# Optimization experiments

Hardware: AMD Instinct MI355X
Metric: run time of the kernel (lower is better)

Reference implementation:

```python
import jax, jax.numpy as jnp
import numpy as np

N, E, D = 8192, 4096, 256
EDGE_DENSITY = 0.05  # ~410 nodes per hyperedge; guarantees no empty edge


def _layernorm(x, gamma, beta, eps=1e-5):
    mu = jnp.mean(x, axis=-1, keepdims=True)
    var = jnp.mean((x - mu) ** 2, axis=-1, keepdims=True)
    return (x - mu) * jax.lax.rsqrt(var + eps) * gamma + beta


def setup_inputs() -> dict:
    key = jax.random.key(0)
    k1, k2, k3 = jax.random.split(key, 3)
    node_embeddings = jax.random.normal(k1, (N, D), dtype=jnp.float32)
    # scale 1/sqrt(N) keeps two chained NxN matmuls per layer numerically sane
    target_martrix = jax.random.normal(k2, (N, N), dtype=jnp.float32) / np.float32(np.sqrt(N))
    hypergraph_matrix = (jax.random.uniform(k3, (N, E)) < EDGE_DENSITY).astype(jnp.float32)
    ln_gamma = jnp.ones((D,), jnp.float32)
    ln_beta = jnp.zeros((D,), jnp.float32)
    return {
        "node_embeddings": node_embeddings,
        "target_martrix": target_martrix,
        "hypergraph_matrix": hypergraph_matrix,
        "ln_gamma": ln_gamma,
        "ln_beta": ln_beta,
        "num_layers": 3,
    }


def reference(node_embeddings, target_martrix, hypergraph_matrix, ln_gamma, ln_beta, num_layers):
    # --- propagation: num_layers rounds of A @ x then A.T @ (.), residual + LN ---
    last = node_embeddings
    source = node_embeddings
    for _ in range(num_layers):
        t = target_martrix @ last            # [N, D]
        source = target_martrix.T @ t        # [N, D]  (pre-residual, pre-norm)
        last = _layernorm(source + node_embeddings, ln_gamma, ln_beta)
        # dropout p=0.35 is identity in eval mode
    # --- hyperedge masked-mean + global max (the torch per-edge python loop) ---
    # NOTE: torch loop uses `source_embedding` of the LAST layer (pre-norm).
    Hb = (hypergraph_matrix > 0).astype(source.dtype)   # [N, E]
    sums = Hb.T @ source                                 # [E, D] segment sums
    counts = jnp.sum(Hb, axis=0)[:, None]                # [E, 1] (all > 0 by construction)
    means = sums / counts                                # per-edge masked mean
    return jnp.max(means, axis=0)                        # [D]
```

## Files before the change

### kernel.cpp

```cpp
#include <hip/hip_runtime.h>


typedef __bf16 bf16;
typedef __bf16 bf16x8 __attribute__((ext_vector_type(8)));
typedef float f32x4 __attribute__((ext_vector_type(4)));

__device__ __forceinline__ void gld_lds16(const bf16* g, bf16* l) {
  __builtin_amdgcn_global_load_lds(
      (const __attribute__((address_space(1))) unsigned int*)g,
      (__attribute__((address_space(3))) unsigned int*)l, 16, 0, 0);
}

template <int BN>
__global__ __launch_bounds__(512) void gemm_bt(const bf16* __restrict__ A,
                                               const bf16* __restrict__ B,
                                               float* __restrict__ P,
                                               int N, int K, int Ks) {
  constexpr int BM = 256, BK = 64;
  constexpr int WM = 64, WN = BN / 2;
  constexpr int TM = WM / 16, TN = WN / 16;
  constexpr int QA = BM / 64, QB = BN / 64;

  __shared__ __align__(16) bf16 As[2][BM * BK];
  __shared__ __align__(16) bf16 Bs[2][BN * BK];

  const int t = threadIdx.x, w = t >> 6, l = t & 63;
  const int srow = l >> 3;
  const int schunk = (l & 7) ^ srow;
  const int n0 = blockIdx.x * BN;
  const int kbase = blockIdx.z * Ks;

  const bf16* gA = A + (size_t)(w * 8 + srow) * K + kbase + schunk * 8;
  const bf16* gB = B + (size_t)(n0 + w * 8 + srow) * K + kbase + schunk * 8;

  auto stage = [&](int kk, int buf) {
    const size_t ko = (size_t)kk * BK;
#pragma unroll
    for (int q = 0; q < QA; ++q)
      gld_lds16(gA + (size_t)(q * 64) * K + ko,
                &As[buf][(q * 64 + w * 8) * BK]);
#pragma unroll
    for (int q = 0; q < QB; ++q)
      gld_lds16(gB + (size_t)(q * 64) * K + ko,
                &Bs[buf][(q * 64 + w * 8) * BK]);
  };

  const int lm = l & 15, kq = l >> 4;
  const int wm = (w >> 1) * WM;
  const int wn = (w & 1) * WN;

  f32x4 acc[TM][TN] = {};
  const int nk = Ks / BK;

  stage(0, 0);
  __syncthreads();

  for (int kk = 0; kk < nk; ++kk) {
    const int buf = kk & 1;
    if (kk + 1 < nk) stage(kk + 1, buf ^ 1);
#pragma unroll
    for (int ks = 0; ks < 2; ++ks) {
      const int csw = ((ks * 4 + kq) ^ (lm & 7)) * 8;
      bf16x8 af[TM], bfr[TN];
#pragma unroll
      for (int i = 0; i < TM; ++i)
        af[i] = *(const bf16x8*)(&As[buf][(wm + i * 16 + lm) * BK + csw]);
#pragma unroll
      for (int j = 0; j < TN; ++j)
        bfr[j] = *(const bf16x8*)(&Bs[buf][(wn + j * 16 + lm) * BK + csw]);
#pragma unroll
      for (int i = 0; i < TM; ++i)
#pragma unroll
        for (int j = 0; j < TN; ++j)
          acc[i][j] = __builtin_amdgcn_mfma_f32_16x16x32_bf16(af[i], bfr[j],
                                                              acc[i][j], 0, 0, 0);
    }
    __syncthreads();
  }

  float* Pz = P + (size_t)blockIdx.z * BM * N;
#pragma unroll
  for (int i = 0; i < TM; ++i) {
    const int mrow = wm + i * 16 + kq * 4;
#pragma unroll
    for (int j = 0; j < TN; ++j) {
      const int col = n0 + wn + j * 16 + lm;
#pragma unroll
      for (int r = 0; r < 4; ++r)
        Pz[(size_t)(mrow + r) * N + col] = acc[i][j][r];
    }
  }
}

__global__ __launch_bounds__(256) void reduce4_bf16(const float* __restrict__ P,
                                                    bf16* __restrict__ out,
                                                    size_t MN) {
  const size_t i4 = ((size_t)blockIdx.x * 256 + threadIdx.x) * 4;
  if (i4 >= MN) return;
  f32x4 a = *(const f32x4*)(P + i4);
  f32x4 b = *(const f32x4*)(P + MN + i4);
  f32x4 c = *(const f32x4*)(P + 2 * MN + i4);
  f32x4 d = *(const f32x4*)(P + 3 * MN + i4);
  a = a + b + c + d;
  bf16 o[4] = {(bf16)a[0], (bf16)a[1], (bf16)a[2], (bf16)a[3]};
  *(int2*)(out + i4) = *(const int2*)o;
}

__global__ __launch_bounds__(256) void transpose_conv(
    const float* __restrict__ src, int R, int C, bf16* __restrict__ cpy,
    bf16* __restrict__ trb, float* __restrict__ trf, float* __restrict__ cnt) {
  __shared__ float tile[64][65];
  __shared__ float cs[4][64];
  const int t = threadIdx.x;
  const int col = t & 63, rb4 = t >> 6;
  const int r0 = blockIdx.y * 64, c0 = blockIdx.x * 64;
  float csum = 0.f;
#pragma unroll
  for (int rr = 0; rr < 64; rr += 4) {
    const int row = rr + rb4;
    const float v = src[(size_t)(r0 + row) * C + c0 + col];
    tile[row][col] = v;
    csum += v;
    if (cpy) cpy[(size_t)(r0 + row) * C + c0 + col] = (bf16)v;
  }
  __syncthreads();
  if (cnt) {
    cs[rb4][col] = csum;
    __syncthreads();
    if (rb4 == 0)
      atomicAdd(&cnt[c0 + col], cs[0][col] + cs[1][col] + cs[2][col] + cs[3][col]);
  }
#pragma unroll
  for (int rr = 0; rr < 64; rr += 4) {
    const int row = rr + rb4;
    const float v = tile[col][row];
    const size_t di = (size_t)(c0 + row) * R + r0 + col;
    if (trb) trb[di] = (bf16)v;
    if (trf) trf[di] = v;
  }
}

__global__ __launch_bounds__(256) void ln_kernel(const float* __restrict__ P,
                                                 const float* __restrict__ x0t,
                                                 const float* __restrict__ gamma,
                                                 const float* __restrict__ beta,
                                                 bf16* __restrict__ Xt) {
  constexpr size_t MN = (size_t)256 * 8192;
  const int tx = threadIdx.x;
  const int ty = threadIdx.y;
  const int i = blockIdx.x * 32 + tx;
  float vbuf[32];
  float s = 0.f, s2 = 0.f;
#pragma unroll
  for (int dd = 0; dd < 32; ++dd) {
    const int d = ty * 32 + dd;
    const size_t idx = (size_t)d * 8192 + i;
    const float v = P[idx] + P[MN + idx] + P[2 * MN + idx] + P[3 * MN + idx] +
                    x0t[idx];
    vbuf[dd] = v;
    s += v;
    s2 += v * v;
  }
  __shared__ float S[8][32], Q[8][32];
  S[ty][tx] = s;
  Q[ty][tx] = s2;
  __syncthreads();
  __shared__ float MU[32], RS[32];
  if (ty == 0) {
    float a = 0.f, b = 0.f;
#pragma unroll
    for (int r = 0; r < 8; ++r) {
      a += S[r][tx];
      b += Q[r][tx];
    }
    const float mu = a * (1.0f / 256.0f);
    const float var = b * (1.0f / 256.0f) - mu * mu;
    MU[tx] = mu;
    RS[tx] = rsqrtf(var + 1e-5f);
  }
  __syncthreads();
  const float mu = MU[tx], rs = RS[tx];
#pragma unroll
  for (int dd = 0; dd < 32; ++dd) {
    const int d = ty * 32 + dd;
    const float y = (vbuf[dd] - mu) * rs * gamma[d] + beta[d];
    Xt[(size_t)d * 8192 + i] = (bf16)y;
  }
}

__global__ __launch_bounds__(256) void final_max(const float* __restrict__ P,
                                                 const float* __restrict__ cnt,
                                                 float* __restrict__ out,
                                                 int S) {
  constexpr size_t MN = (size_t)256 * 4096;
  const int d = blockIdx.x;
  float m = -3.4e38f;
  for (int e = threadIdx.x; e < 4096; e += 256) {
    const size_t idx = (size_t)d * 4096 + e;
    float s = 0.f;
    for (int z = 0; z < S; ++z) s += P[z * MN + idx];
    m = fmaxf(m, s / cnt[e]);
  }
  __shared__ float red[256];
  red[threadIdx.x] = m;
  __syncthreads();
  for (int k = 128; k > 0; k >>= 1) {
    if (threadIdx.x < k)
      red[threadIdx.x] = fmaxf(red[threadIdx.x], red[threadIdx.x + k]);
    __syncthreads();
  }
  if (threadIdx.x == 0) out[d] = red[0];
}

extern "C" void kernel_launch(void* const* d_in, const int* in_sizes, int n_in,
                              void* d_out, int out_size, void* d_ws,
                              size_t ws_size, hipStream_t stream) {
  const float* x0 = (const float*)d_in[0];
  const float* T = (const float*)d_in[1];
  const float* H = (const float*)d_in[2];
  const float* gamma = (const float*)d_in[3];
  const float* beta = (const float*)d_in[4];

  constexpr int Nn = 8192, E = 4096, D = 256, K = 8192;

  char* w = (char*)d_ws;
  size_t off = 0;
  auto carve = [&](size_t bytes) {
    char* p = w + off;
    off += (bytes + 255) & ~(size_t)255;
    return p;
  };
  bf16* Tb = (bf16*)carve((size_t)Nn * Nn * 2);
  bf16* Tt = (bf16*)carve((size_t)Nn * Nn * 2);
  bf16* Htb = (bf16*)carve((size_t)E * Nn * 2);
  float* x0t = (float*)carve((size_t)D * Nn * 4);
  bf16* Xt = (bf16*)carve((size_t)D * Nn * 2);
  bf16* tt = (bf16*)carve((size_t)D * Nn * 2);
  bf16* stb = (bf16*)carve((size_t)D * Nn * 2);
  float* cnts = (float*)carve((size_t)E * 4);
  float* P = (float*)carve((size_t)4 * D * Nn * 4);

  if (off > ws_size) {
    hipMemsetAsync(d_out, 0, (size_t)out_size * 4, stream);
    return;
  }

  hipMemsetAsync(cnts, 0, (size_t)E * 4, stream);
  transpose_conv<<<dim3(128, 128), 256, 0, stream>>>(T, Nn, Nn, Tb, Tt, nullptr,
                                                     nullptr);
  transpose_conv<<<dim3(64, 128), 256, 0, stream>>>(H, Nn, E, nullptr, Htb,
                                                    nullptr, cnts);
  transpose_conv<<<dim3(4, 128), 256, 0, stream>>>(x0, Nn, D, nullptr, Xt, x0t,
                                                   nullptr);

  const size_t MN = (size_t)D * Nn;
  for (int layer = 0; layer < 3; ++layer) {
    gemm_bt<64><<<dim3(128, 1, 4), 512, 0, stream>>>(Xt, Tb, P, Nn, K, K / 4);
    reduce4_bf16<<<(int)(MN / 1024), 256, 0, stream>>>(P, tt, MN);
    gemm_bt<64><<<dim3(128, 1, 4), 512, 0, stream>>>(tt, Tt, P, Nn, K, K / 4);
    if (layer < 2) {
      ln_kernel<<<dim3(256), dim3(32, 8), 0, stream>>>(P, x0t, gamma, beta, Xt);
    } else {
      reduce4_bf16<<<(int)(MN / 1024), 256, 0, stream>>>(P, stb, MN);
    }
  }

  gemm_bt<64><<<dim3(64, 1, 8), 512, 0, stream>>>(stb, Htb, P, E, K, K / 8);
  final_max<<<D, 256, 0, stream>>>(P, cnts, (float*)d_out, 8);
}
```

Before: 1.014 ms.

## Retile split-K GEMM to BK=32, BN=128 with 8-way K split

The bf16 MFMA GEMM changes from BK=64 to BK=32 tiles with a new 4-chunk LDS swizzle and staging pattern. Propagation GEMMs now use BN=128 with an 8-way K split (64x1x8 grid) instead of BN=64 with 4-way. Launch bounds request 2 blocks per CU. The reduce and layernorm kernels now sum 8 fp32 partials, which doubles partial-buffer traffic in exchange for the same block count with larger tiles and possibly higher occupancy.

```diff
diff --git a/kernel.cpp b/kernel.cpp
--- a/kernel.cpp
+++ b/kernel.cpp
@@ -12,42 +12,39 @@
 }
 
 template <int BN>
-__global__ __launch_bounds__(512) void gemm_bt(const bf16* __restrict__ A,
-                                               const bf16* __restrict__ B,
-                                               float* __restrict__ P,
-                                               int N, int K, int Ks) {
-  constexpr int BM = 256, BK = 64;
-  constexpr int WM = 64, WN = BN / 2;
-  constexpr int TM = WM / 16, TN = WN / 16;
-  constexpr int QA = BM / 64, QB = BN / 64;
+__global__ __launch_bounds__(512, 2) void gemm_bt(const bf16* __restrict__ A,
+                                                  const bf16* __restrict__ B,
+                                                  float* __restrict__ P,
+                                                  int N, int K, int Ks) {
+  constexpr int BM = 256, BK = 32;
+  constexpr int WN = BN / 2;
+  constexpr int TM = 4, TN = WN / 16;
 
   __shared__ __align__(16) bf16 As[2][BM * BK];
   __shared__ __align__(16) bf16 Bs[2][BN * BK];
 
   const int t = threadIdx.x, w = t >> 6, l = t & 63;
-  const int srow = l >> 3;
-  const int schunk = (l & 7) ^ srow;
+  const int srow = l >> 2;
+  const int gch = (l & 3) ^ (srow & 3) ^ ((srow >> 2) & 3);
   const int n0 = blockIdx.x * BN;
   const int kbase = blockIdx.z * Ks;
 
-  const bf16* gA = A + (size_t)(w * 8 + srow) * K + kbase + schunk * 8;
-  const bf16* gB = B + (size_t)(n0 + w * 8 + srow) * K + kbase + schunk * 8;
+  const bf16* gA = A + (size_t)(w * 16 + srow) * K + kbase + gch * 8;
+  const bf16* gB = B + (size_t)(n0 + w * 16 + srow) * K + kbase + gch * 8;
 
   auto stage = [&](int kk, int buf) {
     const size_t ko = (size_t)kk * BK;
 #pragma unroll
-    for (int q = 0; q < QA; ++q)
-      gld_lds16(gA + (size_t)(q * 64) * K + ko,
-                &As[buf][(q * 64 + w * 8) * BK]);
-#pragma unroll
-    for (int q = 0; q < QB; ++q)
-      gld_lds16(gB + (size_t)(q * 64) * K + ko,
-                &Bs[buf][(q * 64 + w * 8) * BK]);
+    for (int q = 0; q < 2; ++q)
+      gld_lds16(gA + (size_t)(q * 128) * K + ko,
+                &As[buf][(q * 128 + w * 16) * BK]);
+    if (w < BN / 16) gld_lds16(gB + ko, &Bs[buf][(w * 16) * BK]);
   };
 
   const int lm = l & 15, kq = l >> 4;
-  const int wm = (w >> 1) * WM;
+  const int wm = (w >> 1) * 64;
   const int wn = (w & 1) * WN;
+  const int csw = (kq ^ (lm & 3) ^ ((lm >> 2) & 3)) * 8;
 
   f32x4 acc[TM][TN] = {};
   const int nk = Ks / BK;
@@ -58,23 +55,19 @@
   for (int kk = 0; kk < nk; ++kk) {
     const int buf = kk & 1;
     if (kk + 1 < nk) stage(kk + 1, buf ^ 1);
-#pragma unroll
-    for (int ks = 0; ks < 2; ++ks) {
-      const int csw = ((ks * 4 + kq) ^ (lm & 7)) * 8;
-      bf16x8 af[TM], bfr[TN];
-#pragma unroll
-      for (int i = 0; i < TM; ++i)
-        af[i] = *(const bf16x8*)(&As[buf][(wm + i * 16 + lm) * BK + csw]);
+    bf16x8 af[TM], bfr[TN];
+#pragma unroll
+    for (int i = 0; i < TM; ++i)
+      af[i] = *(const bf16x8*)(&As[buf][(wm + i * 16 + lm) * BK + csw]);
+#pragma unroll
+    for (int j = 0; j < TN; ++j)
+      bfr[j] = *(const bf16x8*)(&Bs[buf][(wn + j * 16 + lm) * BK + csw]);
+#pragma unroll
+    for (int i = 0; i < TM; ++i)
 #pragma unroll
       for (int j = 0; j < TN; ++j)
-        bfr[j] = *(const bf16x8*)(&Bs[buf][(wn + j * 16 + lm) * BK + csw]);
-#pragma unroll
-      for (int i = 0; i < TM; ++i)
-#pragma unroll
-        for (int j = 0; j < TN; ++j)
-          acc[i][j] = __builtin_amdgcn_mfma_f32_16x16x32_bf16(af[i], bfr[j],
-                                                              acc[i][j], 0, 0, 0);
-    }
+        acc[i][j] = __builtin_amdgcn_mfma_f32_16x16x32_bf16(af[i], bfr[j],
+                                                            acc[i][j], 0, 0, 0);
     __syncthreads();
   }
 
@@ -92,16 +85,14 @@
   }
 }
 
-__global__ __launch_bounds__(256) void reduce4_bf16(const float* __restrict__ P,
+__global__ __launch_bounds__(256) void reduce8_bf16(const float* __restrict__ P,
                                                     bf16* __restrict__ out,
                                                     size_t MN) {
   const size_t i4 = ((size_t)blockIdx.x * 256 + threadIdx.x) * 4;
   if (i4 >= MN) return;
-  f32x4 a = *(const f32x4*)(P + i4);
-  f32x4 b = *(const f32x4*)(P + MN + i4);
-  f32x4 c = *(const f32x4*)(P + 2 * MN + i4);
-  f32x4 d = *(const f32x4*)(P + 3 * MN + i4);
-  a = a + b + c + d;
+  f32x4 a = {};
+#pragma unroll
+  for (int z = 0; z < 8; ++z) a += *(const f32x4*)(P + (size_t)z * MN + i4);
   bf16 o[4] = {(bf16)a[0], (bf16)a[1], (bf16)a[2], (bf16)a[3]};
   *(int2*)(out + i4) = *(const int2*)o;
 }
@@ -155,8 +146,9 @@
   for (int dd = 0; dd < 32; ++dd) {
     const int d = ty * 32 + dd;
     const size_t idx = (size_t)d * 8192 + i;
-    const float v = P[idx] + P[MN + idx] + P[2 * MN + idx] + P[3 * MN + idx] +
-                    x0t[idx];
+    float v = x0t[idx];
+#pragma unroll
+    for (int z = 0; z < 8; ++z) v += P[(size_t)z * MN + idx];
     vbuf[dd] = v;
     s += v;
     s2 += v * v;
@@ -238,7 +230,7 @@
   bf16* tt = (bf16*)carve((size_t)D * Nn * 2);
   bf16* stb = (bf16*)carve((size_t)D * Nn * 2);
   float* cnts = (float*)carve((size_t)E * 4);
-  float* P = (float*)carve((size_t)4 * D * Nn * 4);
+  float* P = (float*)carve((size_t)8 * D * Nn * 4);
 
   if (off > ws_size) {
     hipMemsetAsync(d_out, 0, (size_t)out_size * 4, stream);
@@ -255,13 +247,13 @@
 
   const size_t MN = (size_t)D * Nn;
   for (int layer = 0; layer < 3; ++layer) {
-    gemm_bt<64><<<dim3(128, 1, 4), 512, 0, stream>>>(Xt, Tb, P, Nn, K, K / 4);
-    reduce4_bf16<<<(int)(MN / 1024), 256, 0, stream>>>(P, tt, MN);
-    gemm_bt<64><<<dim3(128, 1, 4), 512, 0, stream>>>(tt, Tt, P, Nn, K, K / 4);
+    gemm_bt<128><<<dim3(64, 1, 8), 512, 0, stream>>>(Xt, Tb, P, Nn, K, K / 8);
+    reduce8_bf16<<<(int)(MN / 1024), 256, 0, stream>>>(P, tt, MN);
+    gemm_bt<128><<<dim3(64, 1, 8), 512, 0, stream>>>(tt, Tt, P, Nn, K, K / 8);
     if (layer < 2) {
       ln_kernel<<<dim3(256), dim3(32, 8), 0, stream>>>(P, x0t, gamma, beta, Xt);
     } else {
-      reduce4_bf16<<<(int)(MN / 1024), 256, 0, stream>>>(P, stb, MN);
+      reduce8_bf16<<<(int)(MN / 1024), 256, 0, stream>>>(P, stb, MN);
     }
   }
 
```

Result: slower. 1.109 ms (+9.4%).
